# Optimization experiments

Hardware: AMD Instinct MI355X
Metric: run time of the kernel (lower is better)

The kernel has to match this reference:

```python
import jax, jax.numpy as jnp
import numpy as np

D_MODEL = 512
STATE_DIM = 6
D_STATE = 16
D_CONV = 4
EXPAND = 2
D_INNER = EXPAND * D_MODEL            # 1024
DT_RANK = -(-D_MODEL // 16)           # ceil(d_model/16) = 32


def setup_inputs() -> dict:
    key = jax.random.key(0)
    ks = jax.random.split(key, 12)
    s = 0.02
    return {
        "features": jax.random.normal(ks[0], (32, 2048, D_MODEL), dtype=jnp.float32),
        # Mamba params (mamba_ssm defaults: in/out_proj bias=False, conv+dt_proj bias=True)
        "in_proj_w": jax.random.normal(ks[1], (2 * D_INNER, D_MODEL), dtype=jnp.float32) * s,
        "conv_w": jax.random.normal(ks[2], (D_INNER, D_CONV), dtype=jnp.float32) * s,
        "conv_b": jnp.zeros((D_INNER,), dtype=jnp.float32),
        "x_proj_w": jax.random.normal(ks[3], (DT_RANK + 2 * D_STATE, D_INNER), dtype=jnp.float32) * s,
        "dt_proj_w": jax.random.normal(ks[4], (D_INNER, DT_RANK), dtype=jnp.float32) * s,
        "dt_proj_b": jax.random.normal(ks[5], (D_INNER,), dtype=jnp.float32) * s,
        "A_log": jnp.log(jnp.broadcast_to(jnp.arange(1, D_STATE + 1, dtype=jnp.float32), (D_INNER, D_STATE))),
        "D": jnp.ones((D_INNER,), dtype=jnp.float32),
        "out_proj_w": jax.random.normal(ks[6], (D_MODEL, D_INNER), dtype=jnp.float32) * s,
        # trailing fc head: d_model -> state_dim**2
        "fc_w": jax.random.normal(ks[7], (STATE_DIM * STATE_DIM, D_MODEL), dtype=jnp.float32) * s,
        "fc_b": jnp.zeros((STATE_DIM * STATE_DIM,), dtype=jnp.float32),
    }


def reference(features, in_proj_w, conv_w, conv_b, x_proj_w, dt_proj_w, dt_proj_b,
              A_log, D, out_proj_w, fc_w, fc_b):
    # Original loops Mamba over timesteps with seq_len=1 slices -> each timestep is
    # independent. Flatten (batch, seq) into one token axis and vectorize.
    B_, T, dm = features.shape
    f = features.reshape(B_ * T, dm)                      # (N, d_model)

    xz = f @ in_proj_w.T                                  # (N, 2*d_inner)
    x, z = jnp.split(xz, 2, axis=-1)
    # causal depthwise conv on a length-1 sequence: only the last tap contributes
    x = jax.nn.silu(x * conv_w[:, -1] + conv_b)           # (N, d_inner)

    x_dbl = x @ x_proj_w.T                                # (N, dt_rank + 2*d_state)
    dt = x_dbl[:, :DT_RANK]
    Bm = x_dbl[:, DT_RANK:DT_RANK + D_STATE]              # (N, d_state)
    Cm = x_dbl[:, DT_RANK + D_STATE:]                     # (N, d_state)
    delta = jax.nn.softplus(dt @ dt_proj_w.T + dt_proj_b) # (N, d_inner)

    # single-step selective scan with h0 = 0:
    #   h = exp(delta*A)*0 + delta*B*x ;  y = sum_s C_s h_s + D*x
    # (A_log therefore never affects the output for seq_len=1 calls)
    bc = jnp.sum(Bm * Cm, axis=-1, keepdims=True)         # (N, 1)
    y = delta * x * bc + D * x                            # (N, d_inner)
    y = y * jax.nn.silu(z)

    out = y @ out_proj_w.T                                # (N, d_model)
    A_flat = out @ fc_w.T + fc_b                          # (N, state_dim**2)
    return A_flat.reshape(B_, T, STATE_DIM, STATE_DIM)
```

## Files before the change

kernel.cpp:

```cpp
#include <hip/hip_runtime.h>

typedef unsigned short u16;
typedef unsigned int u32;
typedef __attribute__((ext_vector_type(8))) short bf16x8;
typedef __attribute__((ext_vector_type(4))) float f32x4;

#define NTOK 65536
#define DM 512
#define DI 1024

__device__ __forceinline__ float bf2f(u16 u){ u32 x=((u32)u)<<16; float f; __builtin_memcpy(&f,&x,4); return f; }
__device__ __forceinline__ u16 f2bf(float f){ u32 u; __builtin_memcpy(&u,&f,4); u += 0x7fffu + ((u>>16)&1u); return (u16)(u>>16); }
__device__ __forceinline__ float siluf(float x){ return x/(1.f+__expf(-x)); }
__device__ __forceinline__ float softplus_fast(float x){
  float l = __logf(1.f + __expf(x));
  return (x > 20.f) ? x : l;
}

__device__ __forceinline__ void gload_lds16(const void* g, void* l){
  __builtin_amdgcn_global_load_lds((const __attribute__((address_space(1))) u32*)g,
                                   (__attribute__((address_space(3))) u32*)l, 16, 0, 0);
}

__global__ void k_sentinel(float* out){ out[0] = 1.2345e6f; }

__global__ void k_cast_bf16(const float* __restrict__ in, u16* __restrict__ out, int n){
  int i = (blockIdx.x*256 + threadIdx.x)*4;
  if (i >= n) return;
  float4 v = *(const float4*)(in + i);
  ushort4 o; o.x=f2bf(v.x); o.y=f2bf(v.y); o.z=f2bf(v.z); o.w=f2bf(v.w);
  *(ushort4*)(out + i) = o;
}

__global__ void k_make_wa(const float* __restrict__ fcw, const float* __restrict__ opw,
                          u16* __restrict__ wa){
  int j = blockIdx.x*256 + threadIdx.x;
  int i = blockIdx.y;
  float s = 0.f;
  if (i < 36){
    const float* fr = fcw + i*DM;
    #pragma unroll 8
    for (int k=0;k<DM;++k) s += fr[k]*opw[(size_t)k*DI + j];
  }
  wa[(size_t)i*DI + j] = f2bf(s);
}

__global__ __launch_bounds__(256) void k_gemm_xz(
  const u16* __restrict__ A, const u16* __restrict__ B,
  const float* __restrict__ convw, const float* __restrict__ convb,
  u16* __restrict__ xp, u16* __restrict__ zs)
{
  __shared__ u16 smem[32768];
  u16* SA = smem;
  u16* SB = smem + 16384;
  const int tid=threadIdx.x, wv=tid>>6, ln=tid&63;
  const int l15=ln&15, l4=ln>>4, h=l15&7;
  const int c0g=blockIdx.x*128, r0=blockIdx.y*128;
  const int wm=wv>>1, wn=wv&1;
  const int sr=ln>>3, scs=((ln&7)^sr)*8;
  const int chk0=(l4^h)*8, chk1=((l4+4)^h)*8;
  const int rA=(wm*64+l15)*64, rB=(wn*64+l15)*64;
  f32x4 acc[4][4]={};

  auto STAGE=[&](int buf, int k0){
    u16* Ad = SA + buf*8192;
    u16* Bd = SB + buf*8192;
    #pragma unroll
    for (int it=0;it<4;++it){
      int c=wv*4+it;
      gload_lds16(A + (size_t)(r0 + c*8 + sr)*DM + k0 + scs, Ad + c*512);
    }
    #pragma unroll
    for (int it=0;it<4;++it){
      int c=wv*4+it;
      gload_lds16(B + (size_t)(c0g + c*8 + sr)*DM + k0 + scs, Bd + c*512);
    }
  };

  STAGE(0, 0);
  __syncthreads();
  __builtin_amdgcn_sched_barrier(0);
  int cur = 0;
  #pragma clang loop unroll(disable)
  for (int t=0;t<8;++t){
    if (t < 7) STAGE(cur^1, (t+1)*64);
    const u16* Ac = SA + cur*8192;
    const u16* Bc = SB + cur*8192;
    #pragma unroll
    for (int kk=0;kk<2;++kk){
      const int ch = kk ? chk1 : chk0;
      bf16x8 af[4], bfr[4];
      #pragma unroll
      for (int m=0;m<4;++m) af[m]=*(const bf16x8*)(Ac + rA + m*1024 + ch);
      #pragma unroll
      for (int n=0;n<4;++n) bfr[n]=*(const bf16x8*)(Bc + rB + n*1024 + ch);
      #pragma unroll
      for (int m=0;m<4;++m)
        #pragma unroll
        for (int n=0;n<4;++n)
          acc[m][n]=__builtin_amdgcn_mfma_f32_16x16x32_bf16(af[m],bfr[n],acc[m][n],0,0,0);
    }
    __syncthreads();
    __builtin_amdgcn_sched_barrier(0);
    cur ^= 1;
  }

  const bool isx = (c0g < DI);
  const int cc0 = isx ? c0g : c0g - DI;
  u16* ep = smem;
  #pragma unroll
  for (int n=0;n<4;++n){
    int tcol = wn*64 + n*16 + l15;
    int gcol = c0g + tcol;
    float cw = isx ? convw[gcol*4+3] : 0.f;
    float cb = isx ? convb[gcol]     : 0.f;
    #pragma unroll
    for (int m=0;m<4;++m){
      int trow = wm*64 + m*16 + l4*4;
      #pragma unroll
      for (int r=0;r<4;++r){
        float v = acc[m][n][r];
        float o = isx ? siluf(v*cw + cb) : siluf(v);
        ep[(trow+r)*160 + tcol] = f2bf(o);
      }
    }
  }
  __syncthreads();
  int rrow = tid>>1, half = tid&1;
  const u16* srcp = ep + rrow*160 + half*64;
  u16* dst = (isx ? xp : zs) + (size_t)(r0+rrow)*DI + cc0 + half*64;
  #pragma unroll
  for (int j=0;j<8;++j)
    *(int4*)(dst + j*8) = *(const int4*)(srcp + j*8);
}

__global__ __launch_bounds__(256) void k_gemm_n64(
  const u16* __restrict__ A, const u16* __restrict__ B,
  u16* __restrict__ dtb, float* __restrict__ bc)
{
  __shared__ u16 smem[24576];
  u16* SA = smem;
  u16* SB = smem + 16384;
  const int tid=threadIdx.x, wv=tid>>6, ln=tid&63;
  const int l15=ln&15, l4=ln>>4, h=l15&7;
  const int r0=blockIdx.x*128;
  const int wm=wv>>1, wn=wv&1;
  const int sr=ln>>3, scs=((ln&7)^sr)*8;
  const int chk0=(l4^h)*8, chk1=((l4+4)^h)*8;
  const int rA=(wm*64+l15)*64, rB=(wn*32+l15)*64;
  f32x4 acc[4][2]={};

  auto STAGE=[&](int buf, int k0){
    u16* Ad = SA + buf*8192;
    u16* Bd = SB + buf*4096;
    #pragma unroll
    for (int it=0;it<4;++it){
      int c=wv*4+it;
      gload_lds16(A + (size_t)(r0 + c*8 + sr)*DI + k0 + scs, Ad + c*512);
    }
    #pragma unroll
    for (int it=0;it<2;++it){
      int c=wv*2+it;
      gload_lds16(B + (size_t)(c*8 + sr)*DI + k0 + scs, Bd + c*512);
    }
  };

  STAGE(0, 0);
  __syncthreads();
  __builtin_amdgcn_sched_barrier(0);
  int cur = 0;
  #pragma clang loop unroll(disable)
  for (int t=0;t<16;++t){
    if (t < 15) STAGE(cur^1, (t+1)*64);
    const u16* Ac = SA + cur*8192;
    const u16* Bc = SB + cur*4096;
    #pragma unroll
    for (int kk=0;kk<2;++kk){
      const int ch = kk ? chk1 : chk0;
      bf16x8 af[4], bfr[2];
      #pragma unroll
      for (int m=0;m<4;++m) af[m]=*(const bf16x8*)(Ac + rA + m*1024 + ch);
      #pragma unroll
      for (int n=0;n<2;++n) bfr[n]=*(const bf16x8*)(Bc + rB + n*1024 + ch);
      #pragma unroll
      for (int m=0;m<4;++m)
        #pragma unroll
        for (int n=0;n<2;++n)
          acc[m][n]=__builtin_amdgcn_mfma_f32_16x16x32_bf16(af[m],bfr[n],acc[m][n],0,0,0);
    }
    __syncthreads();
    __builtin_amdgcn_sched_barrier(0);
    cur ^= 1;
  }

  float* W = (float*)smem;
  #pragma unroll
  for (int n=0;n<2;++n){
    int j = wn*32 + n*16 + l15;
    #pragma unroll
    for (int m=0;m<4;++m){
      int trow = wm*64 + m*16 + l4*4;
      #pragma unroll
      for (int r=0;r<4;++r)
        W[(trow+r)*68 + j] = acc[m][n][r];
    }
  }
  __syncthreads();
  const int row = tid>>1, half = tid&1;
  const float* wr = W + row*68;
  if (half==0){
    u16* dst = dtb + (size_t)(r0+row)*32;
    #pragma unroll
    for (int qv=0;qv<4;++qv){
      bf16x8 o;
      #pragma unroll
      for (int e=0;e<8;++e) o[e] = (short)f2bf(wr[qv*8+e]);
      *(bf16x8*)(dst + qv*8) = o;
    }
  } else {
    float s=0.f;
    #pragma unroll
    for (int e=0;e<16;++e) s += wr[32+e]*wr[48+e];
    bc[r0+row] = s;
  }
}

__global__ __launch_bounds__(256) void k_fused(
  const u16* __restrict__ dtb, const u16* __restrict__ Bw,
  const float* __restrict__ dpb, const float* __restrict__ Dv,
  const float* __restrict__ bc,
  const u16* __restrict__ xp, const u16* __restrict__ zs,
  const u16* __restrict__ wa,
  const float* __restrict__ fcb, float* __restrict__ out)
{
  __shared__ u16 As[4096];
  __shared__ u16 Bs[2][4096];
  __shared__ u16 Y[128*136];
  const int tid=threadIdx.x, wv=tid>>6, ln=tid&63;
  const int l15=ln&15, l4=ln>>4;
  const int r0=blockIdx.x*128;
  const int wm=wv>>1, wn=wv&1;
  const int sr=ln>>2, sc=(ln&3)*8;

  #pragma unroll
  for (int it=0;it<2;++it){
    int c=wv*2+it;
    gload_lds16(dtb + (size_t)(r0 + c*16 + sr)*32 + sc, As + c*512);
  }
  #pragma unroll
  for (int it=0;it<2;++it){
    int c=wv*2+it;
    gload_lds16(Bw + (size_t)(c*16 + sr)*32 + sc, Bs[0] + c*512);
  }
  __syncthreads();
  __builtin_amdgcn_sched_barrier(0);

  bf16x8 af[4];
  #pragma unroll
  for (int m=0;m<4;++m) af[m]=*(const bf16x8*)(As + (wm*64+m*16+l15)*32 + l4*8);

  f32x4 oacc[2][4]={};
  const int yrow = tid>>1, yhalf = tid&1;
  int cur = 0;

  #pragma clang loop unroll(disable)
  for (int ch=0; ch<8; ++ch){
    f32x4 dacc[4][4]={};
    bf16x8 bfr[4];
    #pragma unroll
    for (int n=0;n<4;++n) bfr[n]=*(const bf16x8*)(Bs[cur] + (wn*64+n*16+l15)*32 + l4*8);
    #pragma unroll
    for (int m=0;m<4;++m)
      #pragma unroll
      for (int n=0;n<4;++n)
        dacc[m][n]=__builtin_amdgcn_mfma_f32_16x16x32_bf16(af[m],bfr[n],dacc[m][n],0,0,0);
    if (ch<7){
      #pragma unroll
      for (int it=0;it<2;++it){
        int c=wv*2+it;
        gload_lds16(Bw + (size_t)((ch+1)*128 + c*16 + sr)*32 + sc, Bs[cur^1] + c*512);
      }
    }
    #pragma unroll
    for (int n=0;n<4;++n){
      int tcol = wn*64 + n*16 + l15;
      int j = ch*128 + tcol;
      float dpbj = dpb[j], Dj = Dv[j];
      #pragma unroll
      for (int m=0;m<4;++m){
        int trow = wm*64 + m*16 + l4*4;
        #pragma unroll
        for (int r=0;r<4;++r){
          float delta = softplus_fast(dacc[m][n][r] + dpbj);
          float w = delta*bc[r0 + trow + r] + Dj;
          Y[(trow+r)*136 + tcol] = f2bf(w);
        }
      }
    }
    __syncthreads();
    {
      u16* wp = Y + yrow*136 + yhalf*64;
      const size_t gbase = (size_t)(r0 + yrow)*DI + ch*128 + yhalf*64;
      const u16* xpp = xp + gbase;
      const u16* zp  = zs + gbase;
      #pragma unroll
      for (int q=0;q<8;++q){
        bf16x8 wv8 = *(const bf16x8*)(wp + q*8);
        bf16x8 xv  = *(const bf16x8*)(xpp + q*8);
        bf16x8 zv  = *(const bf16x8*)(zp + q*8);
        bf16x8 ov;
        #pragma unroll
        for (int e=0;e<8;++e){
          float y = bf2f((u16)wv8[e]) * bf2f((u16)xv[e]) * bf2f((u16)zv[e]);
          ov[e] = (short)f2bf(y);
        }
        *(bf16x8*)(wp + q*8) = ov;
      }
    }
    __syncthreads();
    #pragma unroll
    for (int kk=0;kk<4;++kk){
      bf16x8 af2[2], bf2r[4];
      #pragma unroll
      for (int m=0;m<2;++m)
        af2[m]=*(const bf16x8*)(Y + (wv*32 + m*16 + l15)*136 + kk*32 + l4*8);
      #pragma unroll
      for (int n=0;n<4;++n)
        bf2r[n]=*(const bf16x8*)(wa + (size_t)(n*16 + l15)*DI + ch*128 + kk*32 + l4*8);
      #pragma unroll
      for (int m=0;m<2;++m)
        #pragma unroll
        for (int n=0;n<4;++n)
          oacc[m][n]=__builtin_amdgcn_mfma_f32_16x16x32_bf16(af2[m],bf2r[n],oacc[m][n],0,0,0);
    }
    __syncthreads();
    __builtin_amdgcn_sched_barrier(0);
    cur ^= 1;
  }

  #pragma unroll
  for (int n=0;n<4;++n){
    int j = n*16 + l15;
    if (j < 36){
      float fj = fcb[j];
      #pragma unroll
      for (int m=0;m<2;++m){
        #pragma unroll
        for (int r=0;r<4;++r){
          int t = r0 + wv*32 + m*16 + l4*4 + r;
          out[(size_t)t*36 + j] = oacc[m][n][r] + fj;
        }
      }
    }
  }
}

extern "C" void kernel_launch(void* const* d_in, const int* in_sizes, int n_in,
                              void* d_out, int out_size, void* d_ws, size_t ws_size,
                              hipStream_t stream){
  const float* f      = (const float*)d_in[0];
  const float* inpw   = (const float*)d_in[1];
  const float* convw  = (const float*)d_in[2];
  const float* convb  = (const float*)d_in[3];
  const float* xprojw = (const float*)d_in[4];
  const float* dtpw   = (const float*)d_in[5];
  const float* dtpb   = (const float*)d_in[6];
  const float* Dv     = (const float*)d_in[8];
  const float* opw    = (const float*)d_in[9];
  const float* fcw    = (const float*)d_in[10];
  const float* fcb    = (const float*)d_in[11];
  float* out = (float*)d_out;

  char* ws = (char*)d_ws;
  size_t off = 0;
  auto alloc = [&](size_t sz)->void*{ void* p = ws + off; off += (sz + 255) & ~(size_t)255; return p; };
  u16*   fbf = (u16*)  alloc((size_t)NTOK*DM*2);
  u16*   xp  = (u16*)  alloc((size_t)NTOK*DI*2);
  u16*   zy  = (u16*)  alloc((size_t)NTOK*DI*2);
  u16*   dtb = (u16*)  alloc((size_t)NTOK*32*2);
  float* bc  = (float*)alloc((size_t)NTOK*4);
  u16*   ipw = (u16*)  alloc((size_t)2048*512*2);
  u16*   xpw = (u16*)  alloc((size_t)64*1024*2);
  u16*   dpw = (u16*)  alloc((size_t)1024*32*2);
  u16*   wa  = (u16*)  alloc((size_t)64*1024*2);
  if (off > ws_size){ k_sentinel<<<1,1,0,stream>>>(out); return; }

  k_cast_bf16<<<dim3((NTOK*DM/4)/256),256,0,stream>>>(f, fbf, NTOK*DM);
  k_cast_bf16<<<dim3((2048*512/4)/256),256,0,stream>>>(inpw, ipw, 2048*512);
  k_cast_bf16<<<dim3((64*1024/4)/256),256,0,stream>>>(xprojw, xpw, 64*1024);
  k_cast_bf16<<<dim3((1024*32/4)/256),256,0,stream>>>(dtpw, dpw, 1024*32);
  k_make_wa<<<dim3(4,64),256,0,stream>>>(fcw, opw, wa);

  k_gemm_xz<<<dim3(16,512),256,0,stream>>>(fbf, ipw, convw, convb, xp, zy);
  k_gemm_n64<<<dim3(512),256,0,stream>>>(xp, xpw, dtb, bc);
  k_fused<<<dim3(512),256,0,stream>>>(dtb, dpw, dtpb, Dv, bc, xp, zy, wa, fcb, out);
}
```

Baseline: 501.5 us.

## Fuse x_proj GEMM into tail kernel, merge weight casts, remap xz tiles per XCD

```diff
diff --git a/kernel.cpp b/kernel.cpp
--- a/kernel.cpp
+++ b/kernel.cpp
@@ -30,6 +30,20 @@
   float4 v = *(const float4*)(in + i);
   ushort4 o; o.x=f2bf(v.x); o.y=f2bf(v.y); o.z=f2bf(v.z); o.w=f2bf(v.w);
   *(ushort4*)(out + i) = o;
+}
+
+__global__ void k_cast_weights(const float* __restrict__ ipw_f, const float* __restrict__ xpw_f,
+                               const float* __restrict__ dpw_f,
+                               u16* __restrict__ ipw, u16* __restrict__ xpw, u16* __restrict__ dpw){
+  int b = blockIdx.x;
+  const float* src; u16* dst; int base;
+  if (b < 1024){ src=ipw_f; dst=ipw; base = b*1024; }
+  else if (b < 1088){ src=xpw_f; dst=xpw; base = (b-1024)*1024; }
+  else { src=dpw_f; dst=dpw; base = (b-1088)*1024; }
+  int i = base + threadIdx.x*4;
+  float4 v = *(const float4*)(src + i);
+  ushort4 o; o.x=f2bf(v.x); o.y=f2bf(v.y); o.z=f2bf(v.z); o.w=f2bf(v.w);
+  *(ushort4*)(dst + i) = o;
 }
 
 __global__ void k_make_wa(const float* __restrict__ fcw, const float* __restrict__ opw,
@@ -55,7 +69,11 @@
   u16* SB = smem + 16384;
   const int tid=threadIdx.x, wv=tid>>6, ln=tid&63;
   const int l15=ln&15, l4=ln>>4, h=l15&7;
-  const int c0g=blockIdx.x*128, r0=blockIdx.y*128;
+  const int l = blockIdx.y*16 + blockIdx.x;
+  const int xcd = l & 7, q = l >> 3;
+  const int cb = q & 15;
+  const int g  = (q >> 4)*8 + xcd;
+  const int c0g = cb*128, r0 = g*128;
   const int wm=wv>>1, wn=wv&1;
   const int sr=ln>>3, scs=((ln&7)^sr)*8;
   const int chk0=(l4^h)*8, chk1=((l4+4)^h)*8;
@@ -113,14 +131,14 @@
     int tcol = wn*64 + n*16 + l15;
     int gcol = c0g + tcol;
     float cw = isx ? convw[gcol*4+3] : 0.f;
-    float cb = isx ? convb[gcol]     : 0.f;
+    float cb2= isx ? convb[gcol]     : 0.f;
     #pragma unroll
     for (int m=0;m<4;++m){
       int trow = wm*64 + m*16 + l4*4;
       #pragma unroll
       for (int r=0;r<4;++r){
         float v = acc[m][n][r];
-        float o = isx ? siluf(v*cw + cb) : siluf(v);
+        float o = isx ? siluf(v*cw + cb2) : siluf(v);
         ep[(trow+r)*160 + tcol] = f2bf(o);
       }
     }
@@ -134,13 +152,17 @@
     *(int4*)(dst + j*8) = *(const int4*)(srcp + j*8);
 }
 
-__global__ __launch_bounds__(256) void k_gemm_n64(
-  const u16* __restrict__ A, const u16* __restrict__ B,
-  u16* __restrict__ dtb, float* __restrict__ bc)
+__global__ __launch_bounds__(256) void k_tail(
+  const u16* __restrict__ xp, const u16* __restrict__ xpw,
+  const u16* __restrict__ dpw,
+  const float* __restrict__ dpb, const float* __restrict__ Dv,
+  const u16* __restrict__ zs, const u16* __restrict__ wa,
+  const float* __restrict__ fcb, float* __restrict__ out)
 {
-  __shared__ u16 smem[24576];
-  u16* SA = smem;
-  u16* SB = smem + 16384;
+  __shared__ u16 smem[29952];
+  u16*   As  = smem;
+  float* bcs = (float*)(smem + 4096);
+  u16*   S   = smem + 4352;
   const int tid=threadIdx.x, wv=tid>>6, ln=tid&63;
   const int l15=ln&15, l4=ln>>4, h=l15&7;
   const int r0=blockIdx.x*128;
@@ -148,113 +170,93 @@
   const int sr=ln>>3, scs=((ln&7)^sr)*8;
   const int chk0=(l4^h)*8, chk1=((l4+4)^h)*8;
   const int rA=(wm*64+l15)*64, rB=(wn*32+l15)*64;
-  f32x4 acc[4][2]={};
-
-  auto STAGE=[&](int buf, int k0){
-    u16* Ad = SA + buf*8192;
-    u16* Bd = SB + buf*4096;
-    #pragma unroll
-    for (int it=0;it<4;++it){
-      int c=wv*4+it;
-      gload_lds16(A + (size_t)(r0 + c*8 + sr)*DI + k0 + scs, Ad + c*512);
-    }
-    #pragma unroll
-    for (int it=0;it<2;++it){
-      int c=wv*2+it;
-      gload_lds16(B + (size_t)(c*8 + sr)*DI + k0 + scs, Bd + c*512);
-    }
-  };
-
-  STAGE(0, 0);
-  __syncthreads();
-  __builtin_amdgcn_sched_barrier(0);
-  int cur = 0;
-  #pragma clang loop unroll(disable)
-  for (int t=0;t<16;++t){
-    if (t < 15) STAGE(cur^1, (t+1)*64);
-    const u16* Ac = SA + cur*8192;
-    const u16* Bc = SB + cur*4096;
-    #pragma unroll
-    for (int kk=0;kk<2;++kk){
-      const int ch = kk ? chk1 : chk0;
-      bf16x8 af[4], bfr[2];
-      #pragma unroll
-      for (int m=0;m<4;++m) af[m]=*(const bf16x8*)(Ac + rA + m*1024 + ch);
-      #pragma unroll
-      for (int n=0;n<2;++n) bfr[n]=*(const bf16x8*)(Bc + rB + n*1024 + ch);
-      #pragma unroll
-      for (int m=0;m<4;++m)
-        #pragma unroll
-        for (int n=0;n<2;++n)
-          acc[m][n]=__builtin_amdgcn_mfma_f32_16x16x32_bf16(af[m],bfr[n],acc[m][n],0,0,0);
-    }
+  const int sr2=ln>>2, sc2=(ln&3)*8;
+
+  {
+    f32x4 acc[4][2]={};
+    auto STAGE=[&](int buf, int k0){
+      u16* Ad = S + buf*8192;
+      u16* Bd = S + 16384 + buf*4096;
+      #pragma unroll
+      for (int it=0;it<4;++it){
+        int c=wv*4+it;
+        gload_lds16(xp + (size_t)(r0 + c*8 + sr)*DI + k0 + scs, Ad + c*512);
+      }
+      #pragma unroll
+      for (int it=0;it<2;++it){
+        int c=wv*2+it;
+        gload_lds16(xpw + (size_t)(c*8 + sr)*DI + k0 + scs, Bd + c*512);
+      }
+    };
+    STAGE(0, 0);
     __syncthreads();
     __builtin_amdgcn_sched_barrier(0);
-    cur ^= 1;
-  }
-
-  float* W = (float*)smem;
-  #pragma unroll
-  for (int n=0;n<2;++n){
-    int j = wn*32 + n*16 + l15;
-    #pragma unroll
-    for (int m=0;m<4;++m){
-      int trow = wm*64 + m*16 + l4*4;
-      #pragma unroll
-      for (int r=0;r<4;++r)
-        W[(trow+r)*68 + j] = acc[m][n][r];
-    }
-  }
-  __syncthreads();
-  const int row = tid>>1, half = tid&1;
-  const float* wr = W + row*68;
-  if (half==0){
-    u16* dst = dtb + (size_t)(r0+row)*32;
-    #pragma unroll
-    for (int qv=0;qv<4;++qv){
-      bf16x8 o;
-      #pragma unroll
-      for (int e=0;e<8;++e) o[e] = (short)f2bf(wr[qv*8+e]);
-      *(bf16x8*)(dst + qv*8) = o;
-    }
-  } else {
-    float s=0.f;
-    #pragma unroll
-    for (int e=0;e<16;++e) s += wr[32+e]*wr[48+e];
-    bc[r0+row] = s;
-  }
-}
-
-__global__ __launch_bounds__(256) void k_fused(
-  const u16* __restrict__ dtb, const u16* __restrict__ Bw,
-  const float* __restrict__ dpb, const float* __restrict__ Dv,
-  const float* __restrict__ bc,
-  const u16* __restrict__ xp, const u16* __restrict__ zs,
-  const u16* __restrict__ wa,
-  const float* __restrict__ fcb, float* __restrict__ out)
-{
-  __shared__ u16 As[4096];
-  __shared__ u16 Bs[2][4096];
-  __shared__ u16 Y[128*136];
-  const int tid=threadIdx.x, wv=tid>>6, ln=tid&63;
-  const int l15=ln&15, l4=ln>>4;
-  const int r0=blockIdx.x*128;
-  const int wm=wv>>1, wn=wv&1;
-  const int sr=ln>>2, sc=(ln&3)*8;
-
-  #pragma unroll
-  for (int it=0;it<2;++it){
-    int c=wv*2+it;
-    gload_lds16(dtb + (size_t)(r0 + c*16 + sr)*32 + sc, As + c*512);
-  }
-  #pragma unroll
-  for (int it=0;it<2;++it){
-    int c=wv*2+it;
-    gload_lds16(Bw + (size_t)(c*16 + sr)*32 + sc, Bs[0] + c*512);
-  }
-  __syncthreads();
-  __builtin_amdgcn_sched_barrier(0);
-
+    int cur = 0;
+    #pragma clang loop unroll(disable)
+    for (int t=0;t<16;++t){
+      if (t < 15) STAGE(cur^1, (t+1)*64);
+      const u16* Ac = S + cur*8192;
+      const u16* Bc = S + 16384 + cur*4096;
+      #pragma unroll
+      for (int kk=0;kk<2;++kk){
+        const int ch = kk ? chk1 : chk0;
+        bf16x8 af[4], bfr[2];
+        #pragma unroll
+        for (int m=0;m<4;++m) af[m]=*(const bf16x8*)(Ac + rA + m*1024 + ch);
+        #pragma unroll
+        for (int n=0;n<2;++n) bfr[n]=*(const bf16x8*)(Bc + rB + n*1024 + ch);
+        #pragma unroll
+        for (int m=0;m<4;++m)
+          #pragma unroll
+          for (int n=0;n<2;++n)
+            acc[m][n]=__builtin_amdgcn_mfma_f32_16x16x32_bf16(af[m],bfr[n],acc[m][n],0,0,0);
+      }
+      __syncthreads();
+      __builtin_amdgcn_sched_barrier(0);
+      cur ^= 1;
+    }
+    float* W = (float*)S;
+    #pragma unroll
+    for (int n=0;n<2;++n){
+      int j = wn*32 + n*16 + l15;
+      #pragma unroll
+      for (int m=0;m<4;++m){
+        int trow = wm*64 + m*16 + l4*4;
+        #pragma unroll
+        for (int r=0;r<4;++r)
+          W[(trow+r)*68 + j] = acc[m][n][r];
+      }
+    }
+    __syncthreads();
+    const int row = tid>>1, half = tid&1;
+    const float* wr = W + row*68;
+    if (half==0){
+      #pragma unroll
+      for (int qv=0;qv<4;++qv){
+        bf16x8 o;
+        #pragma unroll
+        for (int e=0;e<8;++e) o[e] = (short)f2bf(wr[qv*8+e]);
+        *(bf16x8*)(As + row*32 + qv*8) = o;
+      }
+    } else {
+      float s=0.f;
+      #pragma unroll
+      for (int e=0;e<16;++e) s += wr[32+e]*wr[48+e];
+      bcs[row] = s;
+    }
+    {
+      u16* Bs0 = S + 17408;
+      #pragma unroll
+      for (int it=0;it<2;++it){
+        int c=wv*2+it;
+        gload_lds16(dpw + (size_t)(c*16 + sr2)*32 + sc2, Bs0 + c*512);
+      }
+    }
+    __syncthreads();
+  }
+
+  u16* Y   = S;
+  u16* BsB = S + 17408;
   bf16x8 af[4];
   #pragma unroll
   for (int m=0;m<4;++m) af[m]=*(const bf16x8*)(As + (wm*64+m*16+l15)*32 + l4*8);
@@ -268,7 +270,7 @@
     f32x4 dacc[4][4]={};
     bf16x8 bfr[4];
     #pragma unroll
-    for (int n=0;n<4;++n) bfr[n]=*(const bf16x8*)(Bs[cur] + (wn*64+n*16+l15)*32 + l4*8);
+    for (int n=0;n<4;++n) bfr[n]=*(const bf16x8*)(BsB + cur*4096 + (wn*64+n*16+l15)*32 + l4*8);
     #pragma unroll
     for (int m=0;m<4;++m)
       #pragma unroll
@@ -278,7 +280,7 @@
       #pragma unroll
       for (int it=0;it<2;++it){
         int c=wv*2+it;
-        gload_lds16(Bw + (size_t)((ch+1)*128 + c*16 + sr)*32 + sc, Bs[cur^1] + c*512);
+        gload_lds16(dpw + (size_t)((ch+1)*128 + c*16 + sr2)*32 + sc2, BsB + (cur^1)*4096 + c*512);
       }
     }
     #pragma unroll
@@ -292,7 +294,7 @@
         #pragma unroll
         for (int r=0;r<4;++r){
           float delta = softplus_fast(dacc[m][n][r] + dpbj);
-          float w = delta*bc[r0 + trow + r] + Dj;
+          float w = delta*bcs[trow + r] + Dj;
           Y[(trow+r)*136 + tcol] = f2bf(w);
         }
       }
@@ -304,17 +306,17 @@
       const u16* xpp = xp + gbase;
       const u16* zp  = zs + gbase;
       #pragma unroll
-      for (int q=0;q<8;++q){
-        bf16x8 wv8 = *(const bf16x8*)(wp + q*8);
-        bf16x8 xv  = *(const bf16x8*)(xpp + q*8);
-        bf16x8 zv  = *(const bf16x8*)(zp + q*8);
+      for (int qq=0;qq<8;++qq){
+        bf16x8 wv8 = *(const bf16x8*)(wp + qq*8);
+        bf16x8 xv  = *(const bf16x8*)(xpp + qq*8);
+        bf16x8 zv  = *(const bf16x8*)(zp + qq*8);
         bf16x8 ov;
         #pragma unroll
         for (int e=0;e<8;++e){
           float y = bf2f((u16)wv8[e]) * bf2f((u16)xv[e]) * bf2f((u16)zv[e]);
           ov[e] = (short)f2bf(y);
         }
-        *(bf16x8*)(wp + q*8) = ov;
+        *(bf16x8*)(wp + qq*8) = ov;
       }
     }
     __syncthreads();
@@ -377,8 +379,6 @@
   u16*   fbf = (u16*)  alloc((size_t)NTOK*DM*2);
   u16*   xp  = (u16*)  alloc((size_t)NTOK*DI*2);
   u16*   zy  = (u16*)  alloc((size_t)NTOK*DI*2);
-  u16*   dtb = (u16*)  alloc((size_t)NTOK*32*2);
-  float* bc  = (float*)alloc((size_t)NTOK*4);
   u16*   ipw = (u16*)  alloc((size_t)2048*512*2);
   u16*   xpw = (u16*)  alloc((size_t)64*1024*2);
   u16*   dpw = (u16*)  alloc((size_t)1024*32*2);
@@ -386,12 +386,9 @@
   if (off > ws_size){ k_sentinel<<<1,1,0,stream>>>(out); return; }
 
   k_cast_bf16<<<dim3((NTOK*DM/4)/256),256,0,stream>>>(f, fbf, NTOK*DM);
-  k_cast_bf16<<<dim3((2048*512/4)/256),256,0,stream>>>(inpw, ipw, 2048*512);
-  k_cast_bf16<<<dim3((64*1024/4)/256),256,0,stream>>>(xprojw, xpw, 64*1024);
-  k_cast_bf16<<<dim3((1024*32/4)/256),256,0,stream>>>(dtpw, dpw, 1024*32);
+  k_cast_weights<<<dim3(1120),256,0,stream>>>(inpw, xprojw, dtpw, ipw, xpw, dpw);
   k_make_wa<<<dim3(4,64),256,0,stream>>>(fcw, opw, wa);
 
   k_gemm_xz<<<dim3(16,512),256,0,stream>>>(fbf, ipw, convw, convb, xp, zy);
-  k_gemm_n64<<<dim3(512),256,0,stream>>>(xp, xpw, dtb, bc);
-  k_fused<<<dim3(512),256,0,stream>>>(dtb, dpw, dtpb, Dv, bc, xp, zy, wa, fcb, out);
-}
+  k_tail<<<dim3(512),256,0,stream>>>(xp, xpw, dpw, dtpb, Dv, zy, wa, fcb, out);
+}
```

Measured after the change: 467.5 us (median of 3 runs). -6.8%, faster.
